# Kernel tuning notes

Hardware: AMD Instinct MI355X
Metric: run time of the kernel (lower is better)

The kernel has to match this reference:

```python
import jax, jax.numpy as jnp
import numpy as np

GRID_NUM = 28
IMG_SIZE = 224.0
GRID_SIZE = IMG_SIZE / GRID_NUM
LAMBDA_COORD = 5.0
LAMBDA_NOOBJ = 0.5
NUM_CLASSES = 20
EPS = 1e-12


def setup_inputs() -> dict:
    key = jax.random.key(0)
    k1, k2, k3 = jax.random.split(key, 3)
    B, S = 1024, GRID_NUM
    y_pred = jax.random.uniform(k1, (B, S, S, 30), dtype=jnp.float32)
    # y_true channel 0: class id in {0..20}; 0 means no object. channels 1:5: (x, y, w, h)
    cls = jax.random.randint(k2, (B, S, S, 1), 0, NUM_CLASSES + 1).astype(jnp.float32)
    box = jax.random.uniform(k3, (B, S, S, 4), dtype=jnp.float32)
    y_true = jnp.concatenate([cls, box], axis=-1)
    return {"y_pred": y_pred, "y_true": y_true}


def _corners(box, gi, gj):
    # box[..., 0:2] are cell-relative center offsets, box[..., 2:4] are image-relative w/h
    cx = (gj + box[..., 0]) * GRID_SIZE
    cy = (gi + box[..., 1]) * GRID_SIZE
    w = box[..., 2] * IMG_SIZE
    h = box[..., 3] * IMG_SIZE
    return cx - w / 2, cy - h / 2, cx + w / 2, cy + h / 2


def _iou(box_a, box_b, gi, gj):
    ax1, ay1, ax2, ay2 = _corners(box_a, gi, gj)
    bx1, by1, bx2, by2 = _corners(box_b, gi, gj)
    iw = jnp.maximum(jnp.minimum(ax2, bx2) - jnp.maximum(ax1, bx1), 0.0)
    ih = jnp.maximum(jnp.minimum(ay2, by2) - jnp.maximum(ay1, by1), 0.0)
    inter = iw * ih
    area_a = jnp.maximum(ax2 - ax1, 0.0) * jnp.maximum(ay2 - ay1, 0.0)
    area_b = jnp.maximum(bx2 - bx1, 0.0) * jnp.maximum(by2 - by1, 0.0)
    return inter / (area_a + area_b - inter + EPS)


def reference(y_pred, y_true):
    B, S = y_pred.shape[0], y_pred.shape[1]
    gi = jnp.arange(S, dtype=jnp.float32)[None, :, None]  # broadcast over (B, S, S)
    gj = jnp.arange(S, dtype=jnp.float32)[None, None, :]

    obj_mask = y_true[..., 0] != 0.0  # (B, S, S)
    true_box = y_true[..., 1:5]

    iou0 = _iou(y_pred[..., 0:4], true_box, gi, gj)
    iou1 = _iou(y_pred[..., 5:9], true_box, gi, gj)
    # original: choose 0 iff iou0 > iou1, else 1
    choose1 = ~(iou0 > iou1)

    conf_pred = jnp.where(choose1, y_pred[..., 9], y_pred[..., 4])
    conf_true = jnp.where(choose1, iou1, iou0)
    xy_pred = jnp.where(choose1[..., None], y_pred[..., 5:7], y_pred[..., 0:2])

    loss_conf_obj = jnp.square(conf_pred - conf_true)
    loss_coord = LAMBDA_COORD * jnp.sum(jnp.square(xy_pred - y_true[..., 1:3]), axis=-1)

    cls_idx = y_true[..., 0].astype(jnp.int32) - 1
    cls_onehot = jax.nn.one_hot(cls_idx, NUM_CLASSES, dtype=y_pred.dtype)
    loss_cls = jnp.sum(jnp.square(y_pred[..., 10:] - cls_onehot), axis=-1)

    loss_conf_noobj = LAMBDA_NOOBJ * (jnp.square(y_pred[..., 4]) + jnp.square(y_pred[..., 9]))

    bsz = jnp.float32(B)
    loss_confidence = jnp.sum(jnp.where(obj_mask, loss_conf_obj, loss_conf_noobj)) / bsz
    loss_coordinate = jnp.sum(jnp.where(obj_mask, loss_coord, 0.0)) / bsz
    loss_classification = jnp.sum(jnp.where(obj_mask, loss_cls, 0.0)) / bsz
    return loss_confidence + loss_coordinate + loss_classification
```

## Files before the change

### kernel.cpp

```cpp
#include <hip/hip_runtime.h>


#define S_GRID 28
#define N_CELLS (1024 * S_GRID * S_GRID)
#define CPW 64
#define WPB 4
#define BLOCK (WPB * 64)
#define N_WAVES (N_CELLS / CPW)
#define NBLOCKS (N_WAVES / WPB)

__device__ __forceinline__ float iou_calc(float bx, float by, float bw, float bh,
                                          float tx, float ty, float tw, float th,
                                          float gi, float gj) {
    float acx = (gj + bx) * 8.0f;
    float acy = (gi + by) * 8.0f;
    float aw  = bw * 224.0f;
    float ah  = bh * 224.0f;
    float ax1 = acx - aw * 0.5f, ax2 = acx + aw * 0.5f;
    float ay1 = acy - ah * 0.5f, ay2 = acy + ah * 0.5f;
    float bcx = (gj + tx) * 8.0f;
    float bcy = (gi + ty) * 8.0f;
    float btw = tw * 224.0f;
    float bth = th * 224.0f;
    float bx1 = bcx - btw * 0.5f, bx2 = bcx + btw * 0.5f;
    float by1 = bcy - bth * 0.5f, by2 = bcy + bth * 0.5f;

    float iw = fmaxf(fminf(ax2, bx2) - fmaxf(ax1, bx1), 0.0f);
    float ih = fmaxf(fminf(ay2, by2) - fmaxf(ay1, by1), 0.0f);
    float inter = iw * ih;
    float area_a = fmaxf(ax2 - ax1, 0.0f) * fmaxf(ay2 - ay1, 0.0f);
    float area_b = fmaxf(bx2 - bx1, 0.0f) * fmaxf(by2 - by1, 0.0f);
    return inter / (area_a + area_b - inter + 1e-12f);
}

__global__ __launch_bounds__(BLOCK, 4) void yolo_loss_kernel(const float2* __restrict__ yp2,
                                                             const float* __restrict__ yt,
                                                             float* __restrict__ partials) {
    __shared__ float sp[WPB][CPW * 30];

    int tid  = threadIdx.x;
    int lane = tid & 63;
    int wave = tid >> 6;
    int gwave = blockIdx.x * WPB + wave;

    const float2* pb = yp2 + (size_t)gwave * (CPW * 30 / 2);
    float2 v[15];
#pragma unroll
    for (int k = 0; k < 15; ++k) v[k] = pb[k * 64 + lane];

    float2* spw2 = (float2*)sp[wave];
#pragma unroll
    for (int k = 0; k < 15; ++k) spw2[k * 64 + lane] = v[k];

    int cell = gwave * CPW + lane;
    const float* t = yt + (size_t)cell * 5;
    float tc = t[0], tx = t[1], ty = t[2], tw = t[3], th = t[4];

    float pr[30];
    const float* p = sp[wave] + lane * 30;
#pragma unroll
    for (int k = 0; k < 30; ++k) pr[k] = p[k];

    int ij = cell % (S_GRID * S_GRID);
    float gi = (float)(ij / S_GRID);
    float gj = (float)(ij % S_GRID);

    float iou0 = iou_calc(pr[0], pr[1], pr[2], pr[3], tx, ty, tw, th, gi, gj);
    float iou1 = iou_calc(pr[5], pr[6], pr[7], pr[8], tx, ty, tw, th, gi, gj);
    bool choose1 = !(iou0 > iou1);

    float conf_pred = choose1 ? pr[9] : pr[4];
    float conf_true = choose1 ? iou1 : iou0;
    float xp = choose1 ? pr[5] : pr[0];
    float yp = choose1 ? pr[6] : pr[1];

    float dcf = conf_pred - conf_true;
    float d0 = xp - tx, d1 = yp - ty;

    int cls = (int)tc - 1;
    float lcls = 0.0f;
#pragma unroll
    for (int k = 0; k < 20; ++k) {
        float oh = (k == cls) ? 1.0f : 0.0f;
        float d = pr[10 + k] - oh;
        lcls += d * d;
    }

    float obj_loss   = dcf * dcf + 5.0f * (d0 * d0 + d1 * d1) + lcls;
    float noobj_loss = 0.5f * (pr[4] * pr[4] + pr[9] * pr[9]);
    float val = (tc != 0.0f) ? obj_loss : noobj_loss;

#pragma unroll
    for (int off = 32; off > 0; off >>= 1) {
        val += __shfl_down(val, off, 64);
    }
    if (lane == 0) partials[gwave] = val;
}

__global__ __launch_bounds__(256) void reduce_kernel(const float* __restrict__ partials,
                                                     float* __restrict__ out) {
    int tid = threadIdx.x;
    float s = 0.0f;
#pragma unroll
    for (int k = 0; k < 49; ++k) {
        s += partials[k * 256 + tid];
    }
#pragma unroll
    for (int off = 32; off > 0; off >>= 1) {
        s += __shfl_down(s, off, 64);
    }
    __shared__ float wsum[4];
    int lane = tid & 63;
    int wid  = tid >> 6;
    if (lane == 0) wsum[wid] = s;
    __syncthreads();
    if (tid == 0) {
        out[0] = (wsum[0] + wsum[1] + wsum[2] + wsum[3]) * (1.0f / 1024.0f);
    }
}

extern "C" void kernel_launch(void* const* d_in, const int* in_sizes, int n_in,
                              void* d_out, int out_size, void* d_ws, size_t ws_size,
                              hipStream_t stream) {
    const float2* y_pred = (const float2*)d_in[0];
    const float*  y_true = (const float*)d_in[1];
    float* out = (float*)d_out;
    float* partials = (float*)d_ws;

    yolo_loss_kernel<<<NBLOCKS, BLOCK, 0, stream>>>(y_pred, y_true, partials);
    reduce_kernel<<<1, 256, 0, stream>>>(partials, out);
}
```

Baseline: 152.5 us.

## Persistent waves with double-buffered async global-to-LDS loads

Replaces one-tile-per-wave launches with a fixed grid of 1024 blocks of 2 waves that loop over tiles. Each wave prefetches the next tile of y_pred and y_true straight into LDS with global_load_lds while it computes the current tile, which is meant to hide memory latency and skip the register round trip. y_true is now staged through LDS as well, and the final reduction shrinks to 2048 partials. The cost is manual vmcnt waits that depend on the exact number of issued loads, and fewer resident waves per CU.

```diff
diff --git a/kernel.cpp b/kernel.cpp
--- a/kernel.cpp
+++ b/kernel.cpp
@@ -4,10 +4,38 @@
 #define S_GRID 28
 #define N_CELLS (1024 * S_GRID * S_GRID)
 #define CPW 64
-#define WPB 4
+#define N_TILES (N_CELLS / CPW)
+#define WPB 2
 #define BLOCK (WPB * 64)
-#define N_WAVES (N_CELLS / CPW)
-#define NBLOCKS (N_WAVES / WPB)
+#define NBLOCKS 1024
+#define NWAVES (NBLOCKS * WPB)
+
+typedef unsigned int u32;
+
+__device__ __forceinline__ void async16(const float* g, float* l) {
+    __builtin_amdgcn_global_load_lds((const __attribute__((address_space(1))) u32*)g,
+                                     (__attribute__((address_space(3))) u32*)l, 16, 0, 0);
+}
+__device__ __forceinline__ void async4(const float* g, float* l) {
+    __builtin_amdgcn_global_load_lds((const __attribute__((address_space(1))) u32*)g,
+                                     (__attribute__((address_space(3))) u32*)l, 4, 0, 0);
+}
+
+__device__ __forceinline__ void stage(const float* __restrict__ yp,
+                                      const float* __restrict__ yt,
+                                      int tile, int lane,
+                                      float* spred, float* syt) {
+    const float* gp = yp + (size_t)tile * (CPW * 30);
+#pragma unroll
+    for (int j = 0; j < 7; ++j)
+        async16(gp + j * 256 + lane * 4, spred + j * 256);
+    async4(gp + 1792 + lane, spred + 1792);
+    async4(gp + 1856 + lane, spred + 1856);
+    const float* gt = yt + (size_t)tile * (CPW * 5);
+#pragma unroll
+    for (int j = 0; j < 5; ++j)
+        async4(gt + j * 64 + lane, syt + j * 64);
+}
 
 __device__ __forceinline__ float iou_calc(float bx, float by, float bw, float bh,
                                           float tx, float ty, float tw, float th,
@@ -33,68 +61,86 @@
     return inter / (area_a + area_b - inter + 1e-12f);
 }
 
-__global__ __launch_bounds__(BLOCK, 4) void yolo_loss_kernel(const float2* __restrict__ yp2,
+__global__ __launch_bounds__(BLOCK, 2) void yolo_loss_kernel(const float* __restrict__ yp,
                                                              const float* __restrict__ yt,
                                                              float* __restrict__ partials) {
-    __shared__ float sp[WPB][CPW * 30];
+    __shared__ __align__(16) float sp[WPB][2][CPW * 30];
+    __shared__ __align__(16) float sy[WPB][2][CPW * 5];
 
     int tid  = threadIdx.x;
     int lane = tid & 63;
     int wave = tid >> 6;
     int gwave = blockIdx.x * WPB + wave;
 
-    const float2* pb = yp2 + (size_t)gwave * (CPW * 30 / 2);
-    float2 v[15];
+    float acc = 0.0f;
+    int buf = 0;
+
+    stage(yp, yt, gwave, lane, sp[wave][0], sy[wave][0]);
+
+    for (int t = gwave; t < N_TILES; t += NWAVES) {
+        int tn = t + NWAVES;
+        if (tn < N_TILES) {
+            stage(yp, yt, tn, lane, sp[wave][buf ^ 1], sy[wave][buf ^ 1]);
+            asm volatile("s_waitcnt vmcnt(14)" ::: "memory");
+        } else {
+            asm volatile("s_waitcnt vmcnt(0)" ::: "memory");
+        }
+
+        const float* spw = sp[wave][buf];
+        const float* syw = sy[wave][buf];
+
+        const float2* p2 = (const float2*)(spw + lane * 30);
+        float pr[30];
 #pragma unroll
-    for (int k = 0; k < 15; ++k) v[k] = pb[k * 64 + lane];
+        for (int k = 0; k < 15; ++k) {
+            float2 q = p2[k];
+            pr[2 * k]     = q.x;
+            pr[2 * k + 1] = q.y;
+        }
+        float tc = syw[lane * 5 + 0];
+        float tx = syw[lane * 5 + 1];
+        float ty = syw[lane * 5 + 2];
+        float tw = syw[lane * 5 + 3];
+        float th = syw[lane * 5 + 4];
 
-    float2* spw2 = (float2*)sp[wave];
+        int cell = t * CPW + lane;
+        int ij = cell % (S_GRID * S_GRID);
+        float gi = (float)(ij / S_GRID);
+        float gj = (float)(ij % S_GRID);
+
+        float iou0 = iou_calc(pr[0], pr[1], pr[2], pr[3], tx, ty, tw, th, gi, gj);
+        float iou1 = iou_calc(pr[5], pr[6], pr[7], pr[8], tx, ty, tw, th, gi, gj);
+        bool choose1 = !(iou0 > iou1);
+
+        float conf_pred = choose1 ? pr[9] : pr[4];
+        float conf_true = choose1 ? iou1 : iou0;
+        float xp  = choose1 ? pr[5] : pr[0];
+        float ypv = choose1 ? pr[6] : pr[1];
+
+        float dcf = conf_pred - conf_true;
+        float d0 = xp - tx, d1 = ypv - ty;
+
+        int cls = (int)tc - 1;
+        float lcls = 0.0f;
 #pragma unroll
-    for (int k = 0; k < 15; ++k) spw2[k * 64 + lane] = v[k];
+        for (int k = 0; k < 20; ++k) {
+            float oh = (k == cls) ? 1.0f : 0.0f;
+            float d = pr[10 + k] - oh;
+            lcls += d * d;
+        }
 
-    int cell = gwave * CPW + lane;
-    const float* t = yt + (size_t)cell * 5;
-    float tc = t[0], tx = t[1], ty = t[2], tw = t[3], th = t[4];
+        float obj_loss   = dcf * dcf + 5.0f * (d0 * d0 + d1 * d1) + lcls;
+        float noobj_loss = 0.5f * (pr[4] * pr[4] + pr[9] * pr[9]);
+        acc += (tc != 0.0f) ? obj_loss : noobj_loss;
 
-    float pr[30];
-    const float* p = sp[wave] + lane * 30;
-#pragma unroll
-    for (int k = 0; k < 30; ++k) pr[k] = p[k];
-
-    int ij = cell % (S_GRID * S_GRID);
-    float gi = (float)(ij / S_GRID);
-    float gj = (float)(ij % S_GRID);
-
-    float iou0 = iou_calc(pr[0], pr[1], pr[2], pr[3], tx, ty, tw, th, gi, gj);
-    float iou1 = iou_calc(pr[5], pr[6], pr[7], pr[8], tx, ty, tw, th, gi, gj);
-    bool choose1 = !(iou0 > iou1);
-
-    float conf_pred = choose1 ? pr[9] : pr[4];
-    float conf_true = choose1 ? iou1 : iou0;
-    float xp = choose1 ? pr[5] : pr[0];
-    float yp = choose1 ? pr[6] : pr[1];
-
-    float dcf = conf_pred - conf_true;
-    float d0 = xp - tx, d1 = yp - ty;
-
-    int cls = (int)tc - 1;
-    float lcls = 0.0f;
-#pragma unroll
-    for (int k = 0; k < 20; ++k) {
-        float oh = (k == cls) ? 1.0f : 0.0f;
-        float d = pr[10 + k] - oh;
-        lcls += d * d;
+        buf ^= 1;
     }
-
-    float obj_loss   = dcf * dcf + 5.0f * (d0 * d0 + d1 * d1) + lcls;
-    float noobj_loss = 0.5f * (pr[4] * pr[4] + pr[9] * pr[9]);
-    float val = (tc != 0.0f) ? obj_loss : noobj_loss;
 
 #pragma unroll
     for (int off = 32; off > 0; off >>= 1) {
-        val += __shfl_down(val, off, 64);
+        acc += __shfl_down(acc, off, 64);
     }
-    if (lane == 0) partials[gwave] = val;
+    if (lane == 0) partials[gwave] = acc;
 }
 
 __global__ __launch_bounds__(256) void reduce_kernel(const float* __restrict__ partials,
@@ -102,7 +148,7 @@
     int tid = threadIdx.x;
     float s = 0.0f;
 #pragma unroll
-    for (int k = 0; k < 49; ++k) {
+    for (int k = 0; k < 8; ++k) {
         s += partials[k * 256 + tid];
     }
 #pragma unroll
@@ -122,8 +168,8 @@
 extern "C" void kernel_launch(void* const* d_in, const int* in_sizes, int n_in,
                               void* d_out, int out_size, void* d_ws, size_t ws_size,
                               hipStream_t stream) {
-    const float2* y_pred = (const float2*)d_in[0];
-    const float*  y_true = (const float*)d_in[1];
+    const float* y_pred = (const float*)d_in[0];
+    const float* y_true = (const float*)d_in[1];
     float* out = (float*)d_out;
     float* partials = (float*)d_ws;
 
```

Result: no change. 153.3 us (+0.5%).
